# Kernel optimization log

Measured on AMD Instinct MI355X. Metric: run time of the kernel, lower is better.

## Reference

```python
import jax, jax.numpy as jnp
import numpy as np

# Dimensions
T, B = 128, 512
NTOK, NINP, NHID = 512, 512, 600
NB, BS, TOPK = 6, 100, 4          # num_blocks, block_size = nhid//num_blocks, update_topk
H, DK, DV, ATT = 4, 64, 85, 340   # input-attention heads, key dim, value dim (H*DV == attention_out)
H2, DK2, DV2 = 4, 32, 32          # communication (step) attention dims


def setup_inputs() -> dict:
    key = jax.random.key(0)
    ks = jax.random.split(key, 16)
    def rn(k, shape, s=0.05):
        return (jax.random.normal(k, shape) * s).astype(jnp.float32)
    return dict(
        input=jax.random.normal(ks[0], (T, B, NTOK), dtype=jnp.float32),
        h0=jnp.zeros((B, NHID), jnp.float32),
        masks=jnp.ones((T, B, 1), jnp.float32),
        enc_W=rn(ks[1], (NTOK, NINP)), enc_b=jnp.zeros((NINP,), jnp.float32),
        Wq_in=rn(ks[2], (BS, H * DK)), Wk_in=rn(ks[3], (NINP, H * DK)), Wv_in=rn(ks[4], (NINP, H * DV)),
        W_ih=rn(ks[5], (NB, ATT, 3 * BS)), W_hh=rn(ks[6], (NB, BS, 3 * BS)),
        b_ih=jnp.zeros((NB, 3 * BS), jnp.float32), b_hh=jnp.zeros((NB, 3 * BS), jnp.float32),
        Wq_c=rn(ks[7], (BS, H2 * DK2)), Wk_c=rn(ks[8], (BS, H2 * DK2)),
        Wv_c=rn(ks[9], (BS, H2 * DV2)), Wo_c=rn(ks[10], (H2 * DV2, BS)),
        dec_W=rn(ks[11], (NHID, NTOK)), dec_b=jnp.zeros((NTOK,), jnp.float32),
    )


def _rim_scan(emb, masks, h0, Wq_in, Wk_in, Wv_in, W_ih, W_hh, b_ih, b_hh,
              Wq_c, Wk_c, Wv_c, Wo_c):
    inv_sdk = 1.0 / np.sqrt(DK).astype(np.float32)
    inv_sdk2 = 1.0 / np.sqrt(DK2).astype(np.float32)

    def step(h, xm):
        xt, mt = xm                      # [B,NINP], [B,1]
        h = h * mt                       # episode-reset gating
        hb = h.reshape(B, NB, BS)
        # --- input attention over {real input, null} slots ---
        slots = jnp.stack([xt, jnp.zeros_like(xt)], axis=1)          # [B,2,NINP]
        k = (slots @ Wk_in).reshape(B, 2, H, DK)
        v = (slots @ Wv_in).reshape(B, 2, H, DV)
        q = (hb @ Wq_in).reshape(B, NB, H, DK)
        att = jax.nn.softmax(jnp.einsum('bnhd,bshd->bnhs', q, k) * inv_sdk, axis=-1)
        act = 1.0 - att[..., 1].mean(-1)                             # [B,NB] attention to real input
        kth = jax.lax.top_k(act, TOPK)[0][:, -1:]
        mask = (act >= kth).astype(h.dtype)                          # [B,NB] top-k block activation
        inp_use = jnp.einsum('bnhs,bshd->bnhd', att, v).reshape(B, NB, ATT)
        # --- block-diagonal GRU update ---
        gi = jnp.einsum('bnd,nde->bne', inp_use, W_ih) + b_ih
        gh = jnp.einsum('bnd,nde->bne', hb, W_hh) + b_hh
        gi_r, gi_z, gi_n = jnp.split(gi, 3, axis=-1)
        gh_r, gh_z, gh_n = jnp.split(gh, 3, axis=-1)
        r = jax.nn.sigmoid(gi_r + gh_r)
        z = jax.nn.sigmoid(gi_z + gh_z)
        n = jnp.tanh(gi_n + r * gh_n)
        hn = (1.0 - z) * n + z * hb
        # --- step (communication) attention across blocks, residual ---
        qc = (hn @ Wq_c).reshape(B, NB, H2, DK2)
        kc = (hn @ Wk_c).reshape(B, NB, H2, DK2)
        vc = (hn @ Wv_c).reshape(B, NB, H2, DV2)
        ac = jax.nn.softmax(jnp.einsum('bnhd,bmhd->bhnm', qc, kc) * inv_sdk2, axis=-1)
        co = jnp.einsum('bhnm,bmhd->bnhd', ac, vc).reshape(B, NB, H2 * DV2) @ Wo_c
        hc = hn + co
        # --- only top-k active blocks are updated ---
        m = mask[..., None]
        hf = (m * hc + (1.0 - m) * hb).reshape(B, NHID)
        return hf, (hf, mask)

    h_last, (hs, bmask) = jax.lax.scan(step, h0, (emb, masks))
    return hs, h_last, bmask


def reference(input, h0, masks, enc_W, enc_b, Wq_in, Wk_in, Wv_in,
              W_ih, W_hh, b_ih, b_hh, Wq_c, Wk_c, Wv_c, Wo_c, dec_W, dec_b):
    emb = input @ enc_W + enc_b                                      # encoder Linear [T,B,NINP]
    hs, h_last, bmask = _rim_scan(emb, masks, h0, Wq_in, Wk_in, Wv_in,
                                  W_ih, W_hh, b_ih, b_hh, Wq_c, Wk_c, Wv_c, Wo_c)
    dec = hs @ dec_W + dec_b                                         # decoder [T,B,NTOK]
    return dec
```

## Files before the change

### kernel.cpp

```cpp
#include <hip/hip_runtime.h>
#include <math.h>

#define T_STEPS 128
#define BATCH   512
#define NTOK    512
#define NINP    512
#define NHID    600
#define NBK     6
#define BS      100
#define HH      4
#define DK      64
#define DV      85
#define ATT     340
#define H2      4
#define DK2     32
#define DV2     32
#define G3      300
#define VN      340
#define KAPN    400
#define CN      740
#define CNP     768
#define UN2     1800
#define UN2P    1920
#define UK0     128
#define KV0     512
#define DECKP   640
#define SW      2

typedef __attribute__((ext_vector_type(8))) short short8;
typedef __attribute__((ext_vector_type(4))) float f32x4;

__device__ __forceinline__ float sigf(float x) { return 1.f / (1.f + expf(-x)); }
__device__ __forceinline__ unsigned short f2b(float f) {
    unsigned u = __float_as_uint(f);
    unsigned r = (u + 0x7fffu + ((u >> 16) & 1u)) >> 16;
    return (unsigned short)r;
}
__device__ __forceinline__ float b2f(unsigned short u) {
    return __uint_as_float(((unsigned)u) << 16);
}
__device__ __forceinline__ void split3(float x, unsigned short& hi,
                                       unsigned short& mid, unsigned short& lo) {
    hi = f2b(x);
    float r1 = x - b2f(hi);
    mid = f2b(r1);
    lo = f2b(r1 - b2f(mid));
}

struct ZOff { int div; long s1; long s2; };
__device__ __forceinline__ long zoff(ZOff z, int bz) {
    return (long)(bz / z.div) * z.s1 + (long)(bz % z.div) * z.s2;
}

__global__ __launch_bounds__(256) void gemm6(
    const unsigned short* __restrict__ A, long aZ, int aZdiv,
    const unsigned short* __restrict__ B, long bZ,
    float* __restrict__ C, long cZ, int ldc, int Nreal,
    const float* __restrict__ bias, int K0)
{
    const int z = blockIdx.z;
    A += (long)(z / aZdiv) * aZ;
    B += (long)z * bZ;
    C += (long)z * cZ;
    const int LDA = 3 * K0;
    const int m0 = blockIdx.y * 128, n0 = blockIdx.x * 128;
    __shared__ __align__(16) unsigned short As[128 * 64];
    __shared__ __align__(16) unsigned short Bs[128 * 64];
    const int tid = threadIdx.x;
    const int lane = tid & 63;
    const int wid = tid >> 6;
    const int wr = wid >> 1, wc = wid & 1;

    f32x4 acc[4][4];
#pragma unroll
    for (int m = 0; m < 4; m++)
#pragma unroll
        for (int n = 0; n < 4; n++)
#pragma unroll
            for (int v = 0; v < 4; v++) acc[m][n][v] = 0.f;

    const int segA[6] = {0, 0, 1, 0, 2, 1};
    const int segB[6] = {0, 1, 0, 2, 0, 1};
    for (int p = 0; p < 6; p++) {
        const unsigned short* Ap = A + segA[p] * K0;
        const unsigned short* Bp = B + segB[p] * K0;
        for (int k0 = 0; k0 < K0; k0 += 64) {
            short8 ra[4], rb[4];
#pragma unroll
            for (int q = 0; q < 4; q++) {
                int idx = (q << 8) + tid;
                int r = idx >> 3, ce = (idx & 7) << 3;
                ra[q] = *(const short8*)&Ap[(long)(m0 + r) * LDA + k0 + ce];
                rb[q] = *(const short8*)&Bp[(long)(n0 + r) * LDA + k0 + ce];
            }
            __syncthreads();
#pragma unroll
            for (int q = 0; q < 4; q++) {
                int idx = (q << 8) + tid;
                int r = idx >> 3, ce = (idx & 7) << 3;
                *(short8*)&As[r * 64 + ce] = ra[q];
                *(short8*)&Bs[r * 64 + ce] = rb[q];
            }
            __syncthreads();
#pragma unroll
            for (int kk = 0; kk < 2; kk++) {
                short8 af[4], bfr[4];
#pragma unroll
                for (int m = 0; m < 4; m++)
                    af[m] = *(const short8*)&As[(wr * 64 + m * 16 + (lane & 15)) * 64 + kk * 32 + (lane >> 4) * 8];
#pragma unroll
                for (int n = 0; n < 4; n++)
                    bfr[n] = *(const short8*)&Bs[(wc * 64 + n * 16 + (lane & 15)) * 64 + kk * 32 + (lane >> 4) * 8];
#pragma unroll
                for (int m = 0; m < 4; m++)
#pragma unroll
                    for (int n = 0; n < 4; n++)
                        acc[m][n] = __builtin_amdgcn_mfma_f32_16x16x32_bf16(af[m], bfr[n], acc[m][n], 0, 0, 0);
            }
        }
    }
#pragma unroll
    for (int m = 0; m < 4; m++) {
        int rbase = m0 + wr * 64 + m * 16 + (lane >> 4) * 4;
#pragma unroll
        for (int n = 0; n < 4; n++) {
            int col = n0 + wc * 64 + n * 16 + (lane & 15);
            if (col < Nreal) {
                float bv = bias ? bias[col] : 0.f;
#pragma unroll
                for (int v = 0; v < 4; v++)
                    C[(long)(rbase + v) * ldc + col] = acc[m][n][v] + bv;
            }
        }
    }
}

__global__ __launch_bounds__(256) void gemm_mfma(
    const unsigned short* __restrict__ A,
    const unsigned short* __restrict__ B,
    float* __restrict__ C, int ldc,
    const float* __restrict__ bias, int Kp)
{
    const int m0 = blockIdx.y * 128, n0 = blockIdx.x * 128;
    __shared__ __align__(16) unsigned short As[128 * 64];
    __shared__ __align__(16) unsigned short Bs[128 * 64];
    const int tid = threadIdx.x;
    const int lane = tid & 63;
    const int wid = tid >> 6;
    const int wr = wid >> 1, wc = wid & 1;

    f32x4 acc[4][4];
#pragma unroll
    for (int m = 0; m < 4; m++)
#pragma unroll
        for (int n = 0; n < 4; n++)
#pragma unroll
            for (int v = 0; v < 4; v++) acc[m][n][v] = 0.f;

    for (int k0 = 0; k0 < Kp; k0 += 64) {
        short8 ra[4], rb[4];
#pragma unroll
        for (int q = 0; q < 4; q++) {
            int idx = (q << 8) + tid;
            int r = idx >> 3, ce = (idx & 7) << 3;
            ra[q] = *(const short8*)&A[(long)(m0 + r) * Kp + k0 + ce];
            rb[q] = *(const short8*)&B[(long)(n0 + r) * Kp + k0 + ce];
        }
        __syncthreads();
#pragma unroll
        for (int q = 0; q < 4; q++) {
            int idx = (q << 8) + tid;
            int r = idx >> 3, ce = (idx & 7) << 3;
            *(short8*)&As[r * 64 + ce] = ra[q];
            *(short8*)&Bs[r * 64 + ce] = rb[q];
        }
        __syncthreads();
#pragma unroll
        for (int kk = 0; kk < 2; kk++) {
            short8 af[4], bfr[4];
#pragma unroll
            for (int m = 0; m < 4; m++)
                af[m] = *(const short8*)&As[(wr * 64 + m * 16 + (lane & 15)) * 64 + kk * 32 + (lane >> 4) * 8];
#pragma unroll
            for (int n = 0; n < 4; n++)
                bfr[n] = *(const short8*)&Bs[(wc * 64 + n * 16 + (lane & 15)) * 64 + kk * 32 + (lane >> 4) * 8];
#pragma unroll
            for (int m = 0; m < 4; m++)
#pragma unroll
                for (int n = 0; n < 4; n++)
                    acc[m][n] = __builtin_amdgcn_mfma_f32_16x16x32_bf16(af[m], bfr[n], acc[m][n], 0, 0, 0);
        }
    }
#pragma unroll
    for (int m = 0; m < 4; m++) {
        int rbase = m0 + wr * 64 + m * 16 + (lane >> 4) * 4;
#pragma unroll
        for (int n = 0; n < 4; n++) {
            int col = n0 + wc * 64 + n * 16 + (lane & 15);
            float bv = bias ? bias[col] : 0.f;
#pragma unroll
            for (int v = 0; v < 4; v++)
                C[(long)(rbase + v) * ldc + col] = acc[m][n][v] + bv;
        }
    }
}

__global__ __launch_bounds__(256) void sgemm(
    const float* __restrict__ A, ZOff za, int lda,
    const float* __restrict__ B, ZOff zb, int ldb,
    float* __restrict__ C, ZOff zc, int ldc,
    int M, int N, int K)
{
    const int bz = blockIdx.z;
    A += zoff(za, bz);
    B += zoff(zb, bz);
    C += zoff(zc, bz);
    const int m0 = blockIdx.y * 128, n0 = blockIdx.x * 64;
    __shared__ float As[16][132];
    __shared__ float Bs[16][68];
    const int tid = threadIdx.x;
    const int tm = tid >> 4, tn = tid & 15;
    const int ar = tid >> 1, ak = (tid & 1) * 8;
    const int bk = tid >> 4, bn = (tid & 15) * 4;

    float acc[8][4];
#pragma unroll
    for (int i = 0; i < 8; i++)
#pragma unroll
        for (int j = 0; j < 4; j++) acc[i][j] = 0.f;

    for (int k0 = 0; k0 < K; k0 += 16) {
        float av[8], bv[4];
#pragma unroll
        for (int j = 0; j < 8; j++) {
            int gk = k0 + ak + j;
            av[j] = (gk < K) ? A[(long)(m0 + ar) * lda + gk] : 0.f;
        }
#pragma unroll
        for (int j = 0; j < 4; j++) {
            int gk = k0 + bk, gn = n0 + bn + j;
            bv[j] = (gk < K && gn < N) ? B[(long)gk * ldb + gn] : 0.f;
        }
        __syncthreads();
#pragma unroll
        for (int j = 0; j < 8; j++) As[ak + j][ar] = av[j];
#pragma unroll
        for (int j = 0; j < 4; j++) Bs[bk][bn + j] = bv[j];
        __syncthreads();
#pragma unroll
        for (int kk = 0; kk < 16; kk++) {
            float a[8], b[4];
#pragma unroll
            for (int i = 0; i < 8; i++) a[i] = As[kk][tm * 8 + i];
#pragma unroll
            for (int j = 0; j < 4; j++) b[j] = Bs[kk][tn * 4 + j];
#pragma unroll
            for (int i = 0; i < 8; i++)
#pragma unroll
                for (int j = 0; j < 4; j++)
                    acc[i][j] += a[i] * b[j];
        }
    }
#pragma unroll
    for (int i = 0; i < 8; i++) {
        int gm = m0 + tm * 8 + i;
#pragma unroll
        for (int j = 0; j < 4; j++) {
            int gn = n0 + tn * 4 + j;
            if (gn < N) C[(long)gm * ldc + gn] = acc[i][j];
        }
    }
}

__global__ __launch_bounds__(256) void prep_wqt(const float* __restrict__ Wq_in,
                                                float* __restrict__ WqT)
{
    int idx = blockIdx.x * 256 + threadIdx.x;
    if (idx >= HH * DK * BS) return;
    int h = idx / (DK * BS), r = idx - h * DK * BS, d = r / BS, w = r - d * BS;
    WqT[idx] = Wq_in[w * (HH * DK) + h * DK + d];
}

__global__ __launch_bounds__(256) void bias_k(const float* __restrict__ enc_b,
                                              const float* __restrict__ Wk,
                                              float* __restrict__ kbf)
{
    int j = threadIdx.x;
    if (j >= HH * DK) return;
    float acc = 0.f;
    for (int d = 0; d < NINP; d++) acc += enc_b[d] * Wk[d * (HH * DK) + j];
    kbf[j] = acc;
}

__global__ __launch_bounds__(256) void bias_c_kernel(const float* __restrict__ enc_b,
                                                     const float* __restrict__ Wv,
                                                     const float* __restrict__ kbf,
                                                     const float* __restrict__ WqT,
                                                     float* __restrict__ bias_c)
{
    int j = blockIdx.x * 256 + threadIdx.x;
    if (j >= CNP) return;
    float acc = 0.f;
    if (j < VN) {
        for (int d = 0; d < NINP; d++) acc += enc_b[d] * Wv[d * (HH * DV) + j];
    } else if (j < CN) {
        int r = j - VN;
        int h = r / BS, w = r - h * BS;
        for (int d = 0; d < DK; d++)
            acc += kbf[h * DK + d] * WqT[(h * DK + d) * BS + w];
    }
    bias_c[j] = acc;
}

__global__ __launch_bounds__(256) void cvt_dec(const float* __restrict__ dec_W,
                                               unsigned short* __restrict__ dst)
{
    int idx = blockIdx.x * 256 + threadIdx.x;
    if (idx >= NTOK * DECKP) return;
    int n = idx / DECKP, k = idx - n * DECKP;
    dst[idx] = f2b(k < NHID ? dec_W[k * NTOK + n] : 0.f);
}

__global__ __launch_bounds__(256) void cvt_split_ew(const float* __restrict__ EWfull,
                                                    unsigned short* __restrict__ dst)
{
    int idx = blockIdx.x * 256 + threadIdx.x;
    if (idx >= CNP * NTOK) return;
    int n = idx / NTOK, k = idx - n * NTOK;
    float x = (n < CN) ? EWfull[(long)k * CNP + n] : 0.f;
    unsigned short hi, mid, lo;
    split3(x, hi, mid, lo);
    long base = (long)n * (3 * KV0) + k;
    dst[base] = hi;
    dst[base + KV0] = mid;
    dst[base + 2 * KV0] = lo;
}

__global__ __launch_bounds__(256) void cvt_split_bu2(const float* __restrict__ W_ih,
                                                     unsigned short* __restrict__ dst)
{
    int idx = blockIdx.x * 256 + threadIdx.x;
    if (idx >= HH * UN2P * UK0) return;
    int h = idx / (UN2P * UK0), r = idx - h * (UN2P * UK0);
    int j = r / UK0, kk = r - j * UK0;
    float x = 0.f;
    if (kk < DV && j < UN2) {
        int n = j / G3, e = j - n * G3;
        x = W_ih[((long)n * ATT + h * DV + kk) * G3 + e];
    }
    unsigned short hi, mid, lo;
    split3(x, hi, mid, lo);
    long base = ((long)h * UN2P + j) * (3 * UK0) + kk;
    dst[base] = hi;
    dst[base + UK0] = mid;
    dst[base + 2 * UK0] = lo;
}

__global__ __launch_bounds__(256) void cvt_split_in(const float* __restrict__ src,
                                                    unsigned short* __restrict__ dst, long rows)
{
    long total = rows * NTOK;
    long i = (long)blockIdx.x * 256 + threadIdx.x;
    long stride = (long)gridDim.x * 256;
    for (; i < total; i += stride) {
        long row = i / NTOK; int k = (int)(i - row * NTOK);
        unsigned short hi, mid, lo;
        split3(src[i], hi, mid, lo);
        long base = row * (3 * KV0) + k;
        dst[base] = hi;
        dst[base + KV0] = mid;
        dst[base + 2 * KV0] = lo;
    }
}

__global__ __launch_bounds__(256) void cvt_split_vu(const float* __restrict__ Cbuf,
                                                    unsigned short* __restrict__ dst, int MU)
{
    long total = (long)HH * MU * UK0;
    long i = (long)blockIdx.x * 256 + threadIdx.x;
    long stride = (long)gridDim.x * 256;
    for (; i < total; i += stride) {
        int h = (int)(i / ((long)MU * UK0));
        long r = i - (long)h * MU * UK0;
        long row = r / UK0; int kk = (int)(r - row * UK0);
        float x = (kk < DV) ? Cbuf[row * CNP + h * DV + kk] : 0.f;
        unsigned short hi, mid, lo;
        split3(x, hi, mid, lo);
        long base = ((long)h * MU + row) * (3 * UK0) + kk;
        dst[base] = hi;
        dst[base + UK0] = mid;
        dst[base + 2 * UK0] = lo;
    }
}

__global__ __launch_bounds__(1024) void step_fused(
    const float* __restrict__ h_prev,
    const float* __restrict__ masks_t,
    const float* __restrict__ Cbuf,
    const float* __restrict__ U,
    const float* __restrict__ b_ih, const float* __restrict__ b_hh,
    const float* __restrict__ W_hh,
    const float* __restrict__ Wq_c, const float* __restrict__ Wk_c,
    const float* __restrict__ Wv_c, const float* __restrict__ Wo_c,
    float* __restrict__ h_out,
    unsigned short* __restrict__ A_dec,
    int s_step, int MU)
{
    const int b0 = blockIdx.x * SW, tid = threadIdx.x;
    __shared__ __align__(16) float hbT[NHID][SW];
    __shared__ __align__(16) float hnT[NHID][SW];
    __shared__ __align__(16) float kp[SW][KAPN];
    __shared__ __align__(16) float qcb[SW][768], kcb[SW][768], vcb[SW][768];
    __shared__ __align__(16) float coT[NBK * 128][SW];
    __shared__ float part[SW * 96];
    __shared__ float att[SW][24], mk[SW][NBK];
    __shared__ float lg[SW][144];

    const long rowd0 = (long)s_step * BATCH + b0;

    for (int i = tid; i < SW * NHID; i += 1024) {
        int s = i / NHID, j = i - s * NHID;
        hbT[j][s] = h_prev[(long)(b0 + s) * NHID + j] * masks_t[b0 + s];
    }
    for (int i = tid; i < SW * KAPN; i += 1024) {
        int s = i / KAPN, j = i - s * KAPN;
        kp[s][j] = Cbuf[(rowd0 + s) * CNP + VN + j];
    }
    __syncthreads();
    if (tid < SW * 96) {
        int g = tid >> 2, q = tid & 3;
        int s = g / 24, r = g - s * 24;
        int n = r >> 2, h = r & 3;
        float acc = 0.f;
        int w0 = q * 25;
        for (int w = w0; w < w0 + 25; w++) acc += hbT[n * BS + w][s] * kp[s][h * BS + w];
        part[tid] = acc;
    }
    __syncthreads();
    if (tid < SW * 24) {
        int s = tid / 24, r = tid - s * 24;
        float l = part[tid * 4] + part[tid * 4 + 1] + part[tid * 4 + 2] + part[tid * 4 + 3];
        att[s][r] = sigf(l * 0.125f);
    }
    __syncthreads();
    if (tid < SW) {
        float a[NBK], av[NBK];
        for (int n = 0; n < NBK; n++) {
            av[n] = 0.25f * (att[tid][n * 4] + att[tid][n * 4 + 1] + att[tid][n * 4 + 2] + att[tid][n * 4 + 3]);
            a[n] = av[n];
        }
        for (int i = 0; i < 4; i++) {
            int mx = i;
            for (int j = i + 1; j < NBK; j++) if (a[j] > a[mx]) mx = j;
            float t = a[i]; a[i] = a[mx]; a[mx] = t;
        }
        float kth = a[3];
        for (int n = 0; n < NBK; n++) mk[tid][n] = (av[n] >= kth) ? 1.f : 0.f;
    }

    if (tid < 600) {
        const int n2 = tid / 100, w2 = tid - n2 * 100;
        float gi[3][SW], gh[3][SW];
#pragma unroll
        for (int g = 0; g < 3; g++) {
            float bi = b_ih[n2 * G3 + g * BS + w2];
            float bh = b_hh[n2 * G3 + g * BS + w2];
#pragma unroll
            for (int s = 0; s < SW; s++) { gi[g][s] = bi; gh[g][s] = bh; }
        }
#pragma unroll
        for (int h = 0; h < HH; h++) {
            const float* Uh = U + ((long)h * MU + rowd0) * UN2 + n2 * G3;
#pragma unroll
            for (int s = 0; s < SW; s++) {
                float a = att[s][n2 * 4 + h];
#pragma unroll
                for (int g = 0; g < 3; g++)
                    gi[g][s] += a * Uh[(long)s * UN2 + g * BS + w2];
            }
        }
        const float* Wn = W_hh + (long)n2 * BS * G3;
#pragma unroll 4
        for (int d = 0; d < BS; d++) {
            float w0v = Wn[d * G3 + w2];
            float w1v = Wn[d * G3 + BS + w2];
            float w2v = Wn[d * G3 + 2 * BS + w2];
            float2 hv = *(const float2*)&hbT[n2 * BS + d][0];
            gh[0][0] += w0v * hv.x; gh[0][1] += w0v * hv.y;
            gh[1][0] += w1v * hv.x; gh[1][1] += w1v * hv.y;
            gh[2][0] += w2v * hv.x; gh[2][1] += w2v * hv.y;
        }
        float2 hnv;
        {
            float rr0 = sigf(gi[0][0] + gh[0][0]);
            float zz0 = sigf(gi[1][0] + gh[1][0]);
            float ng0 = tanhf(gi[2][0] + rr0 * gh[2][0]);
            hnv.x = (1.f - zz0) * ng0 + zz0 * hbT[n2 * BS + w2][0];
            float rr1 = sigf(gi[0][1] + gh[0][1]);
            float zz1 = sigf(gi[1][1] + gh[1][1]);
            float ng1 = tanhf(gi[2][1] + rr1 * gh[2][1]);
            hnv.y = (1.f - zz1) * ng1 + zz1 * hbT[n2 * BS + w2][1];
        }
        *(float2*)&hnT[n2 * BS + w2][0] = hnv;
    }
    __syncthreads();

    if (tid < 768) {
        const int mat = tid >> 8, r = tid & 255, ng = r >> 7, c = r & 127;
        const float* W = (mat == 0) ? Wq_c : ((mat == 1) ? Wk_c : Wv_c);
        float acc[3][SW];
#pragma unroll
        for (int j = 0; j < 3; j++)
#pragma unroll
            for (int s = 0; s < SW; s++) acc[j][s] = 0.f;
#pragma unroll 4
        for (int d = 0; d < BS; d++) {
            float wv = W[d * 128 + c];
#pragma unroll
            for (int j = 0; j < 3; j++) {
                float2 hv = *(const float2*)&hnT[(ng * 3 + j) * BS + d][0];
                acc[j][0] += wv * hv.x;
                acc[j][1] += wv * hv.y;
            }
        }
        float (*dst)[768] = (mat == 0) ? qcb : ((mat == 1) ? kcb : vcb);
#pragma unroll
        for (int j = 0; j < 3; j++)
#pragma unroll
            for (int s = 0; s < SW; s++)
                dst[s][(ng * 3 + j) * 128 + c] = acc[j][s];
    }
    __syncthreads();

    if (tid < SW * 144) {
        int s = tid / 144, r = tid - s * 144;
        int h = r / 36, r2 = r - h * 36, n = r2 / NBK, m = r2 - n * NBK;
        float sv = 0.f;
#pragma unroll
        for (int e4 = 0; e4 < 8; e4++) {
            f32x4 qv = *(const f32x4*)&qcb[s][n * 128 + h * 32 + e4 * 4];
            f32x4 kv = *(const f32x4*)&kcb[s][m * 128 + h * 32 + e4 * 4];
            sv += qv[0] * kv[0] + qv[1] * kv[1] + qv[2] * kv[2] + qv[3] * kv[3];
        }
        lg[s][r] = sv * 0.17677669529663687f;
    }
    __syncthreads();
    if (tid < SW * 24) {
        int s = tid / 24, r = tid - s * 24;
        float* row = &lg[s][r * NBK];
        float mx = row[0];
        for (int m = 1; m < NBK; m++) mx = fmaxf(mx, row[m]);
        float sv = 0.f;
        for (int m = 0; m < NBK; m++) { row[m] = expf(row[m] - mx); sv += row[m]; }
        float inv = 1.f / sv;
        for (int m = 0; m < NBK; m++) row[m] *= inv;
    }
    __syncthreads();
    for (int idx = tid; idx < SW * 768; idx += 1024) {
        int s = idx / 768, r = idx - s * 768;
        int n = r >> 7, d = r & 127, h = d >> 5;
        float a = 0.f;
#pragma unroll
        for (int m = 0; m < NBK; m++) a += lg[s][h * 36 + n * NBK + m] * vcb[s][m * 128 + d];
        coT[r][s] = a;
    }
    __syncthreads();

    if (tid < 600) {
        const int n2 = tid / 100, w2 = tid - n2 * 100;
        float a0 = 0.f, a1 = 0.f;
#pragma unroll 4
        for (int d = 0; d < 128; d++) {
            float wv = Wo_c[d * BS + w2];
            float2 cv = *(const float2*)&coT[n2 * 128 + d][0];
            a0 += wv * cv.x;
            a1 += wv * cv.y;
        }
        float2 res;
        float hc0 = hnT[n2 * BS + w2][0] + a0;
        float hc1 = hnT[n2 * BS + w2][1] + a1;
        res.x = (mk[0][n2] > 0.5f) ? hc0 : hbT[n2 * BS + w2][0];
        res.y = (mk[1][n2] > 0.5f) ? hc1 : hbT[n2 * BS + w2][1];
        *(float2*)&hbT[n2 * BS + w2][0] = res;
    }
    __syncthreads();
    for (int i = tid; i < SW * NHID; i += 1024) {
        int s = i / NHID, j = i - s * NHID;
        h_out[(long)(b0 + s) * NHID + j] = hbT[j][s];
    }
    for (int i = tid; i < SW * DECKP; i += 1024) {
        int s = i / DECKP, col = i - s * DECKP;
        A_dec[(rowd0 + s) * DECKP + col] = f2b(col < NHID ? hbT[col][s] : 0.f);
    }
}

extern "C" void kernel_launch(void* const* d_in, const int* in_sizes, int n_in,
                              void* d_out, int out_size, void* d_ws, size_t ws_size,
                              hipStream_t stream)
{
    const float* input = (const float*)d_in[0];
    const float* h0    = (const float*)d_in[1];
    const float* masks = (const float*)d_in[2];
    const float* enc_W = (const float*)d_in[3];
    const float* enc_b = (const float*)d_in[4];
    const float* Wq_in = (const float*)d_in[5];
    const float* Wk_in = (const float*)d_in[6];
    const float* Wv_in = (const float*)d_in[7];
    const float* W_ih  = (const float*)d_in[8];
    const float* W_hh  = (const float*)d_in[9];
    const float* b_ih  = (const float*)d_in[10];
    const float* b_hh  = (const float*)d_in[11];
    const float* Wq_c  = (const float*)d_in[12];
    const float* Wk_c  = (const float*)d_in[13];
    const float* Wv_c  = (const float*)d_in[14];
    const float* Wo_c  = (const float*)d_in[15];
    const float* dec_W = (const float*)d_in[16];
    const float* dec_b = (const float*)d_in[17];
    float* out = (float*)d_out;

    const size_t AL = 256;
    auto pad = [&](size_t x) { return (x + AL - 1) & ~(AL - 1); };
    size_t fixedB = pad((size_t)NTOK * CNP * 4)
                  + pad((size_t)NTOK * 256 * 4)
                  + pad((size_t)HH * DK * BS * 4)
                  + pad((size_t)256 * 4)
                  + pad((size_t)CNP * 4)
                  + pad((size_t)CNP * 3 * KV0 * 2)
                  + pad((size_t)HH * UN2P * 3 * UK0 * 2)
                  + pad((size_t)NTOK * DECKP * 2)
                  + 2 * pad((size_t)BATCH * NHID * 4);
    auto perC = [&](int C) {
        size_t MU = (size_t)C * BATCH;
        return pad(MU * 3 * KV0 * 2)
             + pad(MU * CNP * 4)
             + pad((size_t)HH * MU * 3 * UK0 * 2)
             + pad((size_t)HH * MU * UN2 * 4)
             + pad(MU * DECKP * 2);
    };
    int C = 8;
    while (C > 1 && fixedB + perC(C) > ws_size) C >>= 1;
    const int MU = C * BATCH;
    const int NCH = T_STEPS / C;

    char* p = (char*)d_ws;
    auto alloc = [&](size_t bytes) { char* r = p; p += pad(bytes); return r; };
    float*          EWfull = (float*)alloc((size_t)NTOK * CNP * 4);
    float*          EWk    = (float*)alloc((size_t)NTOK * 256 * 4);
    float*          WqT    = (float*)alloc((size_t)HH * DK * BS * 4);
    float*          kbf    = (float*)alloc((size_t)256 * 4);
    float*          bias_c = (float*)alloc((size_t)CNP * 4);
    unsigned short* B_vkap = (unsigned short*)alloc((size_t)CNP * 3 * KV0 * 2);
    unsigned short* B_U    = (unsigned short*)alloc((size_t)HH * UN2P * 3 * UK0 * 2);
    unsigned short* B_dec  = (unsigned short*)alloc((size_t)NTOK * DECKP * 2);
    float*          hA     = (float*)alloc((size_t)BATCH * NHID * 4);
    float*          hB     = (float*)alloc((size_t)BATCH * NHID * 4);
    unsigned short* A_in   = (unsigned short*)alloc((size_t)MU * 3 * KV0 * 2);
    float*          Cbuf   = (float*)alloc((size_t)MU * CNP * 4);
    unsigned short* A_U    = (unsigned short*)alloc((size_t)HH * MU * 3 * UK0 * 2);
    float*          Ubuf   = (float*)alloc((size_t)HH * MU * UN2 * 4);
    unsigned short* A_dec  = (unsigned short*)alloc((size_t)MU * DECKP * 2);

    dim3 blk(256);
    ZOff z0 = {1, 0, 0};

    sgemm<<<dim3(6, 4, 1), blk, 0, stream>>>(
        enc_W, z0, NINP, Wv_in, z0, HH * DV, EWfull, z0, CNP, NTOK, VN, NINP);
    sgemm<<<dim3(4, 4, 1), blk, 0, stream>>>(
        enc_W, z0, NINP, Wk_in, z0, HH * DK, EWk, z0, 256, NTOK, HH * DK, NINP);
    prep_wqt<<<dim3((HH * DK * BS + 255) / 256), blk, 0, stream>>>(Wq_in, WqT);
    sgemm<<<dim3(2, 4, HH), blk, 0, stream>>>(
        EWk, ZOff{1, DK, 0}, 256, WqT, ZOff{1, (long)DK * BS, 0}, BS,
        EWfull + VN, ZOff{1, BS, 0}, CNP, NTOK, BS, DK);
    bias_k<<<dim3(1), blk, 0, stream>>>(enc_b, Wk_in, kbf);
    bias_c_kernel<<<dim3(3), blk, 0, stream>>>(enc_b, Wv_in, kbf, WqT, bias_c);
    cvt_split_ew<<<dim3((CNP * NTOK + 255) / 256), blk, 0, stream>>>(EWfull, B_vkap);
    cvt_split_bu2<<<dim3((HH * UN2P * UK0 + 255) / 256), blk, 0, stream>>>(W_ih, B_U);
    cvt_dec<<<dim3((NTOK * DECKP + 255) / 256), blk, 0, stream>>>(dec_W, B_dec);

    const float* hp = h0;
    float* hbufs[2] = { hA, hB };
    int t = 0;
    for (int c = 0; c < NCH; c++) {
        cvt_split_in<<<dim3(2048), blk, 0, stream>>>(
            input + (size_t)c * MU * NTOK, A_in, MU);
        gemm6<<<dim3(CNP / 128, MU / 128, 1), blk, 0, stream>>>(
            A_in, 0, 1, B_vkap, 0, Cbuf, 0, CNP, CN, bias_c, KV0);
        cvt_split_vu<<<dim3(2048), blk, 0, stream>>>(Cbuf, A_U, MU);
        gemm6<<<dim3(UN2P / 128, MU / 128, HH), blk, 0, stream>>>(
            A_U, (long)MU * 3 * UK0, 1, B_U, (long)UN2P * 3 * UK0,
            Ubuf, (long)MU * UN2, UN2, UN2, nullptr, UK0);
        for (int s = 0; s < C; s++, t++) {
            float* hout = hbufs[t & 1];
            step_fused<<<dim3(BATCH / SW), dim3(1024), 0, stream>>>(
                hp, masks + (size_t)t * BATCH, Cbuf, Ubuf, b_ih, b_hh, W_hh,
                Wq_c, Wk_c, Wv_c, Wo_c, hout, A_dec, s, MU);
            hp = hout;
        }
        gemm_mfma<<<dim3(NTOK / 128, MU / 128, 1), blk, 0, stream>>>(
            A_dec, B_dec, out + (size_t)c * MU * NTOK, NTOK, dec_b, DECKP);
    }
}
```

Baseline: 6.597 ms.

## Fuse value split into projection GEMM epilogue, swizzle GEMM blocks, repack W_hh

A new GEMM, gemm6_kv, writes the value columns straight into the three-way bf16-split A_U buffer and the key columns into a compact Kbuf. This removes the separate cvt_split_vu pass and the full-width Cbuf round trip. Both GEMMs now remap block indices with an XCD-style swizzle. W_hh is repacked once so the per-step recurrence fetches all three gate weights as a single float4 load instead of three strided loads. A risk is that A_U padding columns (kk >= DV) are no longer zero-written, so correctness depends on the workspace or the B padding being zero.

Measured after the change: 6.537 ms. About the same (-0.9%).

```diff
diff --git a/kernel.cpp b/kernel.cpp
--- a/kernel.cpp
+++ b/kernel.cpp
@@ -52,18 +52,28 @@
     return (long)(bz / z.div) * z.s1 + (long)(bz % z.div) * z.s2;
 }
 
+__device__ __forceinline__ void swz_decode(int& x, int& y, int& z) {
+    int gx = gridDim.x, gy = gridDim.y;
+    int flat = (blockIdx.z * gy + blockIdx.y) * gx + blockIdx.x;
+    int nwg = gx * gy * gridDim.z;
+    int per = nwg >> 3;
+    int nf = (flat & 7) * per + (flat >> 3);
+    y = nf % gy; int t2 = nf / gy; x = t2 % gx; z = t2 / gx;
+}
+
 __global__ __launch_bounds__(256) void gemm6(
     const unsigned short* __restrict__ A, long aZ, int aZdiv,
     const unsigned short* __restrict__ B, long bZ,
     float* __restrict__ C, long cZ, int ldc, int Nreal,
     const float* __restrict__ bias, int K0)
 {
-    const int z = blockIdx.z;
-    A += (long)(z / aZdiv) * aZ;
-    B += (long)z * bZ;
-    C += (long)z * cZ;
+    int bx, by, bz;
+    swz_decode(bx, by, bz);
+    A += (long)(bz / aZdiv) * aZ;
+    B += (long)bz * bZ;
+    C += (long)bz * cZ;
     const int LDA = 3 * K0;
-    const int m0 = blockIdx.y * 128, n0 = blockIdx.x * 128;
+    const int m0 = by * 128, n0 = bx * 128;
     __shared__ __align__(16) unsigned short As[128 * 64];
     __shared__ __align__(16) unsigned short Bs[128 * 64];
     const int tid = threadIdx.x;
@@ -130,6 +140,103 @@
 #pragma unroll
                 for (int v = 0; v < 4; v++)
                     C[(long)(rbase + v) * ldc + col] = acc[m][n][v] + bv;
+            }
+        }
+    }
+}
+
+__global__ __launch_bounds__(256) void gemm6_kv(
+    const unsigned short* __restrict__ A,
+    const unsigned short* __restrict__ B,
+    unsigned short* __restrict__ A_U,
+    float* __restrict__ Kbuf,
+    const float* __restrict__ bias, int K0, int MU)
+{
+    int bx, by, bz;
+    swz_decode(bx, by, bz);
+    const int LDA = 3 * K0;
+    const int m0 = by * 128, n0 = bx * 128;
+    __shared__ __align__(16) unsigned short As[128 * 64];
+    __shared__ __align__(16) unsigned short Bs[128 * 64];
+    const int tid = threadIdx.x;
+    const int lane = tid & 63;
+    const int wid = tid >> 6;
+    const int wr = wid >> 1, wc = wid & 1;
+
+    f32x4 acc[4][4];
+#pragma unroll
+    for (int m = 0; m < 4; m++)
+#pragma unroll
+        for (int n = 0; n < 4; n++)
+#pragma unroll
+            for (int v = 0; v < 4; v++) acc[m][n][v] = 0.f;
+
+    const int segA[6] = {0, 0, 1, 0, 2, 1};
+    const int segB[6] = {0, 1, 0, 2, 0, 1};
+    for (int p = 0; p < 6; p++) {
+        const unsigned short* Ap = A + segA[p] * K0;
+        const unsigned short* Bp = B + segB[p] * K0;
+        for (int k0 = 0; k0 < K0; k0 += 64) {
+            short8 ra[4], rb[4];
+#pragma unroll
+            for (int q = 0; q < 4; q++) {
+                int idx = (q << 8) + tid;
+                int r = idx >> 3, ce = (idx & 7) << 3;
+                ra[q] = *(const short8*)&Ap[(long)(m0 + r) * LDA + k0 + ce];
+                rb[q] = *(const short8*)&Bp[(long)(n0 + r) * LDA + k0 + ce];
+            }
+            __syncthreads();
+#pragma unroll
+            for (int q = 0; q < 4; q++) {
+                int idx = (q << 8) + tid;
+                int r = idx >> 3, ce = (idx & 7) << 3;
+                *(short8*)&As[r * 64 + ce] = ra[q];
+                *(short8*)&Bs[r * 64 + ce] = rb[q];
+            }
+            __syncthreads();
+#pragma unroll
+            for (int kk = 0; kk < 2; kk++) {
+                short8 af[4], bfr[4];
+#pragma unroll
+                for (int m = 0; m < 4; m++)
+                    af[m] = *(const short8*)&As[(wr * 64 + m * 16 + (lane & 15)) * 64 + kk * 32 + (lane >> 4) * 8];
+#pragma unroll
+                for (int n = 0; n < 4; n++)
+                    bfr[n] = *(const short8*)&Bs[(wc * 64 + n * 16 + (lane & 15)) * 64 + kk * 32 + (lane >> 4) * 8];
+#pragma unroll
+                for (int m = 0; m < 4; m++)
+#pragma unroll
+                    for (int n = 0; n < 4; n++)
+                        acc[m][n] = __builtin_amdgcn_mfma_f32_16x16x32_bf16(af[m], bfr[n], acc[m][n], 0, 0, 0);
+            }
+        }
+    }
+#pragma unroll
+    for (int m = 0; m < 4; m++) {
+        int rbase = m0 + wr * 64 + m * 16 + (lane >> 4) * 4;
+#pragma unroll
+        for (int n = 0; n < 4; n++) {
+            int col = n0 + wc * 64 + n * 16 + (lane & 15);
+            if (col < CN) {
+                float bv = bias[col];
+                if (col < VN) {
+                    int h = col / DV, kk2 = col - h * DV;
+#pragma unroll
+                    for (int v = 0; v < 4; v++) {
+                        float val = acc[m][n][v] + bv;
+                        unsigned short hi, mid, lo;
+                        split3(val, hi, mid, lo);
+                        long base = ((long)h * MU + (rbase + v)) * (3 * UK0) + kk2;
+                        A_U[base] = hi;
+                        A_U[base + UK0] = mid;
+                        A_U[base + 2 * UK0] = lo;
+                    }
+                } else {
+                    int kc = col - VN;
+#pragma unroll
+                    for (int v = 0; v < 4; v++)
+                        Kbuf[(long)(rbase + v) * KAPN + kc] = acc[m][n][v] + bv;
+                }
             }
         }
     }
@@ -281,6 +388,17 @@
     WqT[idx] = Wq_in[w * (HH * DK) + h * DK + d];
 }
 
+__global__ __launch_bounds__(256) void prep_whh4(const float* __restrict__ W_hh,
+                                                 float* __restrict__ Whh4)
+{
+    int idx = blockIdx.x * 256 + threadIdx.x;
+    if (idx >= NBK * BS * G3) return;
+    int n = idx / (BS * G3), r = idx - n * (BS * G3);
+    int d = r / G3, e = r - d * G3;
+    int g = e / BS, w = e - g * BS;
+    Whh4[(((long)n * BS + d) * BS + w) * 4 + g] = W_hh[idx];
+}
+
 __global__ __launch_bounds__(256) void bias_k(const float* __restrict__ enc_b,
                                               const float* __restrict__ Wk,
                                               float* __restrict__ kbf)
@@ -373,33 +491,13 @@
     }
 }
 
-__global__ __launch_bounds__(256) void cvt_split_vu(const float* __restrict__ Cbuf,
-                                                    unsigned short* __restrict__ dst, int MU)
-{
-    long total = (long)HH * MU * UK0;
-    long i = (long)blockIdx.x * 256 + threadIdx.x;
-    long stride = (long)gridDim.x * 256;
-    for (; i < total; i += stride) {
-        int h = (int)(i / ((long)MU * UK0));
-        long r = i - (long)h * MU * UK0;
-        long row = r / UK0; int kk = (int)(r - row * UK0);
-        float x = (kk < DV) ? Cbuf[row * CNP + h * DV + kk] : 0.f;
-        unsigned short hi, mid, lo;
-        split3(x, hi, mid, lo);
-        long base = ((long)h * MU + row) * (3 * UK0) + kk;
-        dst[base] = hi;
-        dst[base + UK0] = mid;
-        dst[base + 2 * UK0] = lo;
-    }
-}
-
 __global__ __launch_bounds__(1024) void step_fused(
     const float* __restrict__ h_prev,
     const float* __restrict__ masks_t,
-    const float* __restrict__ Cbuf,
+    const float* __restrict__ Kbuf,
     const float* __restrict__ U,
     const float* __restrict__ b_ih, const float* __restrict__ b_hh,
-    const float* __restrict__ W_hh,
+    const float* __restrict__ Whh4,
     const float* __restrict__ Wq_c, const float* __restrict__ Wk_c,
     const float* __restrict__ Wv_c, const float* __restrict__ Wo_c,
     float* __restrict__ h_out,
@@ -424,7 +522,7 @@
     }
     for (int i = tid; i < SW * KAPN; i += 1024) {
         int s = i / KAPN, j = i - s * KAPN;
-        kp[s][j] = Cbuf[(rowd0 + s) * CNP + VN + j];
+        kp[s][j] = Kbuf[(rowd0 + s) * KAPN + j];
     }
     __syncthreads();
     if (tid < SW * 96) {
@@ -479,16 +577,14 @@
                     gi[g][s] += a * Uh[(long)s * UN2 + g * BS + w2];
             }
         }
-        const float* Wn = W_hh + (long)n2 * BS * G3;
+        const f32x4* Wn4 = ((const f32x4*)Whh4) + (long)n2 * BS * BS + w2;
 #pragma unroll 4
         for (int d = 0; d < BS; d++) {
-            float w0v = Wn[d * G3 + w2];
-            float w1v = Wn[d * G3 + BS + w2];
-            float w2v = Wn[d * G3 + 2 * BS + w2];
+            f32x4 wv = Wn4[(long)d * BS];
             float2 hv = *(const float2*)&hbT[n2 * BS + d][0];
-            gh[0][0] += w0v * hv.x; gh[0][1] += w0v * hv.y;
-            gh[1][0] += w1v * hv.x; gh[1][1] += w1v * hv.y;
-            gh[2][0] += w2v * hv.x; gh[2][1] += w2v * hv.y;
+            gh[0][0] += wv[0] * hv.x; gh[0][1] += wv[0] * hv.y;
+            gh[1][0] += wv[1] * hv.x; gh[1][1] += wv[1] * hv.y;
+            gh[2][0] += wv[2] * hv.x; gh[2][1] += wv[2] * hv.y;
         }
         float2 hnv;
         {
@@ -625,6 +721,7 @@
                   + pad((size_t)HH * DK * BS * 4)
                   + pad((size_t)256 * 4)
                   + pad((size_t)CNP * 4)
+                  + pad((size_t)NBK * BS * BS * 4 * 4)
                   + pad((size_t)CNP * 3 * KV0 * 2)
                   + pad((size_t)HH * UN2P * 3 * UK0 * 2)
                   + pad((size_t)NTOK * DECKP * 2)
@@ -632,7 +729,7 @@
     auto perC = [&](int C) {
         size_t MU = (size_t)C * BATCH;
         return pad(MU * 3 * KV0 * 2)
-             + pad(MU * CNP * 4)
+             + pad(MU * KAPN * 4)
              + pad((size_t)HH * MU * 3 * UK0 * 2)
              + pad((size_t)HH * MU * UN2 * 4)
              + pad(MU * DECKP * 2);
@@ -649,13 +746,14 @@
     float*          WqT    = (float*)alloc((size_t)HH * DK * BS * 4);
     float*          kbf    = (float*)alloc((size_t)256 * 4);
     float*          bias_c = (float*)alloc((size_t)CNP * 4);
+    float*          Whh4   = (float*)alloc((size_t)NBK * BS * BS * 4 * 4);
     unsigned short* B_vkap = (unsigned short*)alloc((size_t)CNP * 3 * KV0 * 2);
     unsigned short* B_U    = (unsigned short*)alloc((size_t)HH * UN2P * 3 * UK0 * 2);
     unsigned short* B_dec  = (unsigned short*)alloc((size_t)NTOK * DECKP * 2);
     float*          hA     = (float*)alloc((size_t)BATCH * NHID * 4);
     float*          hB     = (float*)alloc((size_t)BATCH * NHID * 4);
     unsigned short* A_in   = (unsigned short*)alloc((size_t)MU * 3 * KV0 * 2);
-    float*          Cbuf   = (float*)alloc((size_t)MU * CNP * 4);
+    float*          Kbuf   = (float*)alloc((size_t)MU * KAPN * 4);
     unsigned short* A_U    = (unsigned short*)alloc((size_t)HH * MU * 3 * UK0 * 2);
     float*          Ubuf   = (float*)alloc((size_t)HH * MU * UN2 * 4);
     unsigned short* A_dec  = (unsigned short*)alloc((size_t)MU * DECKP * 2);
@@ -668,6 +766,7 @@
     sgemm<<<dim3(4, 4, 1), blk, 0, stream>>>(
         enc_W, z0, NINP, Wk_in, z0, HH * DK, EWk, z0, 256, NTOK, HH * DK, NINP);
     prep_wqt<<<dim3((HH * DK * BS + 255) / 256), blk, 0, stream>>>(Wq_in, WqT);
+    prep_whh4<<<dim3((NBK * BS * G3 + 255) / 256), blk, 0, stream>>>(W_hh, Whh4);
     sgemm<<<dim3(2, 4, HH), blk, 0, stream>>>(
         EWk, ZOff{1, DK, 0}, 256, WqT, ZOff{1, (long)DK * BS, 0}, BS,
         EWfull + VN, ZOff{1, BS, 0}, CNP, NTOK, BS, DK);
@@ -683,16 +782,15 @@
     for (int c = 0; c < NCH; c++) {
         cvt_split_in<<<dim3(2048), blk, 0, stream>>>(
             input + (size_t)c * MU * NTOK, A_in, MU);
-        gemm6<<<dim3(CNP / 128, MU / 128, 1), blk, 0, stream>>>(
-            A_in, 0, 1, B_vkap, 0, Cbuf, 0, CNP, CN, bias_c, KV0);
-        cvt_split_vu<<<dim3(2048), blk, 0, stream>>>(Cbuf, A_U, MU);
+        gemm6_kv<<<dim3(CNP / 128, MU / 128, 1), blk, 0, stream>>>(
+            A_in, B_vkap, A_U, Kbuf, bias_c, KV0, MU);
         gemm6<<<dim3(UN2P / 128, MU / 128, HH), blk, 0, stream>>>(
             A_U, (long)MU * 3 * UK0, 1, B_U, (long)UN2P * 3 * UK0,
             Ubuf, (long)MU * UN2, UN2, UN2, nullptr, UK0);
         for (int s = 0; s < C; s++, t++) {
             float* hout = hbufs[t & 1];
             step_fused<<<dim3(BATCH / SW), dim3(1024), 0, stream>>>(
-                hp, masks + (size_t)t * BATCH, Cbuf, Ubuf, b_ih, b_hh, W_hh,
+                hp, masks + (size_t)t * BATCH, Kbuf, Ubuf, b_ih, b_hh, Whh4,
                 Wq_c, Wk_c, Wv_c, Wo_c, hout, A_dec, s, MU);
             hp = hout;
         }
```
